# Optimization experiments

Hardware: AMD Instinct MI355X
Metric: run time of the kernel (lower is better)

The kernel has to match this reference:

```python
import math
import jax, jax.numpy as jnp
import numpy as np

B, N, CS, CZ, CH, H, PQ, PV = 1, 4096, 512, 128, 64, 16, 4, 8
BQ, BK = 32, 128
NB = N // BQ
CZ4 = CZ // 4
INF = 100000.0
EPS = 1e-8


def quat_to_rot(q):
    w, x, y, z = q[..., 0], q[..., 1], q[..., 2], q[..., 3]
    return jnp.stack([
        jnp.stack([1 - 2 * (y * y + z * z), 2 * (x * y - w * z), 2 * (x * z + w * y)], -1),
        jnp.stack([2 * (x * y + w * z), 1 - 2 * (x * x + z * z), 2 * (y * z - w * x)], -1),
        jnp.stack([2 * (x * z - w * y), 2 * (y * z + w * x), 1 - 2 * (x * x + y * y)], -1),
    ], -2)


def setup_inputs() -> dict:
    key = jax.random.key(0)
    ks = jax.random.split(key, 16)
    s = jax.random.normal(ks[0], (B, N, CS), jnp.float32)
    z = jax.random.normal(ks[1], (B, NB, BQ, BK, CZ), jnp.float32)
    trans = jax.random.normal(ks[2], (B, N, 3), jnp.float32) * 10.0
    quat = jax.random.normal(ks[3], (B, N, 4), jnp.float32)
    quat = quat / jnp.linalg.norm(quat, axis=-1, keepdims=True)
    rots = quat_to_rot(quat)
    s_mask = jnp.ones((B, N), jnp.float32)
    pad = (BK - BQ) // 2  # key window centered on each query block
    key_idx = (jnp.arange(NB)[:, None] * BQ - pad + jnp.arange(BK)[None, :]).astype(jnp.int32)

    def w(k, shp):
        return jax.random.normal(k, shp, jnp.float32) * (1.0 / math.sqrt(shp[0]))

    return {
        's': s, 'z': z, 'trans': trans, 'rots': rots, 's_mask': s_mask, 'key_idx': key_idx,
        'Wq': w(ks[4], (CS, H * CH)), 'Wk': w(ks[5], (CS, H * CH)), 'Wv': w(ks[6], (CS, H * CH)),
        'Wqp': w(ks[7], (CS, H * PQ * 3)), 'Wkvp': w(ks[8], (CS, H * (PQ + PV) * 3)),
        'Wb': w(ks[9], (CZ, H)), 'Wdz': w(ks[10], (CZ, CZ4)),
        'head_weights': jnp.full((H,), float(np.log(np.e - 1.0)), jnp.float32),  # softplus^-1(1)
        'Wout': w(ks[11], (H * (CZ4 + CH + PV * 4), CS)),
        'g_s': jnp.ones((CS,), jnp.float32), 'b_s': jnp.zeros((CS,), jnp.float32),
        'g_z': jnp.ones((CZ,), jnp.float32), 'b_z': jnp.zeros((CZ,), jnp.float32),
    }


def _ln(x, g, b):
    m = jnp.mean(x, -1, keepdims=True)
    v = jnp.mean((x - m) ** 2, -1, keepdims=True)
    return (x - m) * jax.lax.rsqrt(v + 1e-5) * g + b


def _ipa(s, z, trans, rots, s_mask, key_idx, Wq, Wk, Wv, Wqp, Wkvp, Wb, Wdz,
         head_weights, Wout, g_s, b_s, g_z, b_z):
    s_n = _ln(s, g_s, b_s)
    z_n = _ln(z, g_z, b_z)

    valid = (key_idx >= 0) & (key_idx < N)            # [NB, BK]
    idx = jnp.clip(key_idx, 0, N - 1)
    vf = valid.astype(s.dtype)[None]                  # [1, NB, BK]

    def gk(x):  # gather key window: [B,N,...] -> [B,NB,BK,...]
        return x[:, idx]

    sq = s_n.reshape(B, NB, BQ, CS)
    sk = gk(s_n) * vf[..., None]                      # zero-pad out-of-range keys

    tq = trans.reshape(B, NB, BQ, 3)
    rq = rots.reshape(B, NB, BQ, 3, 3)
    tk = gk(trans) * vf[..., None]
    rk = jnp.where(valid[None, :, :, None, None], gk(rots), jnp.eye(3, dtype=rots.dtype))

    q = (sq @ Wq).reshape(B, NB, BQ, H, CH)
    k = (sk @ Wk).reshape(B, NB, BK, H, CH)
    v = (sk @ Wv).reshape(B, NB, BK, H, CH)

    q_pts = (sq @ Wqp).reshape(B, NB, BQ, H * PQ, 3)
    q_pts = jnp.einsum('bnqij,bnqpj->bnqpi', rq, q_pts) + tq[:, :, :, None, :]
    q_pts = q_pts.reshape(B, NB, BQ, H, PQ, 3)

    kv_pts = (sk @ Wkvp).reshape(B, NB, BK, H * (PQ + PV), 3)
    kv_pts = jnp.einsum('bnkij,bnkpj->bnkpi', rk, kv_pts) + tk[:, :, :, None, :]
    kv_pts = kv_pts.reshape(B, NB, BK, H, PQ + PV, 3)
    k_pts, v_pts = kv_pts[..., :PQ, :], kv_pts[..., PQ:, :]

    bias = jnp.einsum('bnqkc,ch->bnqkh', z_n, Wb)
    a = jnp.einsum('bnqhc,bnkhc->bnqkh', q, k) * math.sqrt(1.0 / (3 * CH))
    a = a + math.sqrt(1.0 / 3) * bias

    disp = q_pts[:, :, :, None] - k_pts[:, :, None]   # [B,NB,BQ,BK,H,PQ,3]
    pt_att = jnp.sum(disp ** 2, -1)                   # [B,NB,BQ,BK,H,PQ]
    hw = jax.nn.softplus(head_weights) * math.sqrt(1.0 / (3 * (PQ * 9.0 / 2)))
    pt_att = -0.5 * jnp.sum(pt_att * hw[:, None], -1)  # [B,NB,BQ,BK,H]

    qm = s_mask.reshape(B, NB, BQ)
    km = gk(s_mask) * vf
    amask = INF * (qm[:, :, :, None] * km[:, :, None, :] - 1.0)

    a = a + pt_att + amask[..., None]
    a = jax.nn.softmax(jnp.swapaxes(a, -1, -2), axis=-1)  # [B,NB,BQ,H,BK]

    o = jnp.einsum('bnqhk,bnkhc->bnqhc', a, v).reshape(B, NB, BQ, H * CH)

    o_pt = jnp.einsum('bnqhk,bnkhpc->bnqhpc', a, v_pts)
    o_pt = jnp.einsum('bnqji,bnqhpj->bnqhpi', rq, o_pt - tq[:, :, :, None, None, :])
    o_pt_norm = jnp.sqrt(jnp.sum(o_pt ** 2, -1) + EPS).reshape(B, NB, BQ, H * PV)
    o_pt = o_pt.reshape(B, NB, BQ, H * PV * 3)

    pair_z = z_n @ Wdz                                # [B,NB,BQ,BK,CZ4]
    o_pair = jnp.einsum('bnqhk,bnqkc->bnqhc', a, pair_z).reshape(B, NB, BQ, H * CZ4)

    out = jnp.concatenate([o, o_pt, o_pt_norm, o_pair], -1) @ Wout
    return out.reshape(B, N, CS)


def reference(s, z, trans, rots, s_mask, key_idx, Wq, Wk, Wv, Wqp, Wkvp, Wb, Wdz,
              head_weights, Wout, g_s, b_s, g_z, b_z):
    return _ipa(s, z, trans, rots, s_mask, key_idx, Wq, Wk, Wv, Wqp, Wkvp, Wb, Wdz,
                head_weights, Wout, g_s, b_s, g_z, b_z)
```

## Files before the change

kernel.cpp:

```cpp
#include <hip/hip_runtime.h>
#include <math.h>

#define D_N 4096
#define PROJW 3840
#define OFFK 1024
#define OFFV 2048
#define OFFQP 3072
#define OFFKVP 3264
#define CATW 2048

typedef __bf16 bf16_t;
typedef __bf16 bf16x8 __attribute__((ext_vector_type(8)));
typedef __bf16 bf16x4 __attribute__((ext_vector_type(4)));
typedef float f32x4 __attribute__((ext_vector_type(4)));

__global__ __launch_bounds__(256) void k_wcatT(const float* __restrict__ Wq, const float* __restrict__ Wk,
    const float* __restrict__ Wv, const float* __restrict__ Wqp, const float* __restrict__ Wkvp,
    bf16_t* __restrict__ out)
{
    __shared__ float T[64][65];
    int c0 = blockIdx.x * 64;
    int r0 = blockIdx.y * 64;
    const float* src; int ld, coff;
    if (c0 < 1024)      { src = Wq;   ld = 1024; coff = c0; }
    else if (c0 < 2048) { src = Wk;   ld = 1024; coff = c0 - 1024; }
    else if (c0 < 3072) { src = Wv;   ld = 1024; coff = c0 - 2048; }
    else if (c0 < 3264) { src = Wqp;  ld = 192;  coff = c0 - 3072; }
    else                { src = Wkvp; ld = 576;  coff = c0 - 3264; }
    int tid = threadIdx.x;
    {
        int rr = tid >> 2, cb = (tid & 3) * 16;
        const float* p = src + (size_t)(r0 + rr) * ld + coff + cb;
        #pragma unroll
        for (int i = 0; i < 4; ++i)
            *(float4*)&T[rr][cb + i * 4] = *(const float4*)(p + i * 4);
    }
    __syncthreads();
    {
        int cc = tid >> 2, rb = (tid & 3) * 16;
        bf16_t* o = out + (size_t)(c0 + cc) * 512 + r0 + rb;
        bf16x8 o0, o1;
        #pragma unroll
        for (int j = 0; j < 8; ++j) o0[j] = (bf16_t)T[rb + j][cc];
        #pragma unroll
        for (int j = 0; j < 8; ++j) o1[j] = (bf16_t)T[rb + 8 + j][cc];
        *(bf16x8*)(o) = o0;
        *(bf16x8*)(o + 8) = o1;
    }
}

__global__ __launch_bounds__(256) void t_cvt(const float* __restrict__ in, bf16_t* __restrict__ out,
    int R, int C)
{
    __shared__ float T[64][65];
    int r0 = blockIdx.y * 64, c0 = blockIdx.x * 64;
    int tid = threadIdx.x;
    {
        int rr = tid >> 2;
        int cb = (tid & 3) * 16;
        const float* p = in + (size_t)(r0 + rr) * C + c0 + cb;
        #pragma unroll
        for (int i = 0; i < 4; ++i) {
            float4 v = *(const float4*)(p + i * 4);
            *(float4*)&T[rr][cb + i * 4] = v;
        }
    }
    __syncthreads();
    {
        int cc = tid >> 2;
        int rb = (tid & 3) * 16;
        bf16_t* o = out + (size_t)(c0 + cc) * R + r0 + rb;
        bf16x8 o0, o1;
        #pragma unroll
        for (int j = 0; j < 8; ++j) o0[j] = (bf16_t)T[rb + j][cc];
        #pragma unroll
        for (int j = 0; j < 8; ++j) o1[j] = (bf16_t)T[rb + 8 + j][cc];
        *(bf16x8*)(o) = o0;
        *(bf16x8*)(o + 8) = o1;
    }
}

__global__ __launch_bounds__(256) void k_wz(const float* __restrict__ Wb, const float* __restrict__ Wdz,
    bf16_t* __restrict__ WzT)
{
    int i = blockIdx.x * 256 + threadIdx.x;
    if (i >= 6144) return;
    int j = i >> 7, k = i & 127;
    float v = (j < 16) ? Wb[k * 16 + j] : Wdz[k * 32 + (j - 16)];
    WzT[i] = (bf16_t)v;
}

__global__ __launch_bounds__(64) void k_ln_s(const float* __restrict__ s, const float* __restrict__ g,
    const float* __restrict__ b, bf16_t* __restrict__ out)
{
    int row = blockIdx.x;
    int lane = threadIdx.x;
    const float4* p = (const float4*)(s + (size_t)row * 512);
    float4 v0 = p[lane];
    float4 v1 = p[lane + 64];
    float sum = v0.x + v0.y + v0.z + v0.w + v1.x + v1.y + v1.z + v1.w;
    float sq  = v0.x*v0.x + v0.y*v0.y + v0.z*v0.z + v0.w*v0.w
              + v1.x*v1.x + v1.y*v1.y + v1.z*v1.z + v1.w*v1.w;
    #pragma unroll
    for (int off = 1; off < 64; off <<= 1) {
        sum += __shfl_xor(sum, off);
        sq  += __shfl_xor(sq, off);
    }
    float m = sum * (1.0f / 512.0f);
    float var = sq * (1.0f / 512.0f) - m * m;
    float rs = rsqrtf(var + 1e-5f);
    int c = lane * 4;
    int c2 = 256 + lane * 4;
    bf16x4 r0, r1;
    r0[0] = (bf16_t)((v0.x - m) * rs * g[c+0] + b[c+0]);
    r0[1] = (bf16_t)((v0.y - m) * rs * g[c+1] + b[c+1]);
    r0[2] = (bf16_t)((v0.z - m) * rs * g[c+2] + b[c+2]);
    r0[3] = (bf16_t)((v0.w - m) * rs * g[c+3] + b[c+3]);
    r1[0] = (bf16_t)((v1.x - m) * rs * g[c2+0] + b[c2+0]);
    r1[1] = (bf16_t)((v1.y - m) * rs * g[c2+1] + b[c2+1]);
    r1[2] = (bf16_t)((v1.z - m) * rs * g[c2+2] + b[c2+2]);
    r1[3] = (bf16_t)((v1.w - m) * rs * g[c2+3] + b[c2+3]);
    *(bf16x4*)(out + (size_t)row * 512 + c)  = r0;
    *(bf16x4*)(out + (size_t)row * 512 + c2) = r1;
}

__global__ __launch_bounds__(256) void gemm_bf128(const bf16_t* __restrict__ A, const bf16_t* __restrict__ BT,
    float* __restrict__ C, int M, int N, int K)
{
    __shared__ bf16_t As[128][40];
    __shared__ bf16_t Bs[128][40];
    const int tid = threadIdx.x, lane = tid & 63, w = tid >> 6;
    const int row0 = blockIdx.y * 128, col0 = blockIdx.x * 128;
    const int wr = (w >> 1) * 64, wc = (w & 1) * 64;
    const int srow = tid >> 1, skoff = (tid & 1) * 16;
    const bf16_t* Ap = A + (size_t)(row0 + srow) * K + skoff;
    const bf16_t* Bp = BT + (size_t)(col0 + srow) * K + skoff;
    f32x4 acc[4][4];
    #pragma unroll
    for (int m = 0; m < 4; ++m)
        #pragma unroll
        for (int n = 0; n < 4; ++n) acc[m][n] = (f32x4){0.f,0.f,0.f,0.f};
    for (int k0 = 0; k0 < K; k0 += 32) {
        uint4 a0 = *(const uint4*)(Ap + k0);
        uint4 a1 = *(const uint4*)(Ap + k0 + 8);
        uint4 b0 = *(const uint4*)(Bp + k0);
        uint4 b1 = *(const uint4*)(Bp + k0 + 8);
        __syncthreads();
        *(uint4*)&As[srow][skoff]     = a0;
        *(uint4*)&As[srow][skoff + 8] = a1;
        *(uint4*)&Bs[srow][skoff]     = b0;
        *(uint4*)&Bs[srow][skoff + 8] = b1;
        __syncthreads();
        bf16x8 af[4], bfr[4];
        #pragma unroll
        for (int m = 0; m < 4; ++m) af[m]  = *(const bf16x8*)&As[wr + m*16 + (lane & 15)][(lane >> 4) * 8];
        #pragma unroll
        for (int n = 0; n < 4; ++n) bfr[n] = *(const bf16x8*)&Bs[wc + n*16 + (lane & 15)][(lane >> 4) * 8];
        #pragma unroll
        for (int m = 0; m < 4; ++m)
            #pragma unroll
            for (int n = 0; n < 4; ++n)
                acc[m][n] = __builtin_amdgcn_mfma_f32_16x16x32_bf16(af[m], bfr[n], acc[m][n], 0, 0, 0);
    }
    #pragma unroll
    for (int m = 0; m < 4; ++m)
        #pragma unroll
        for (int n = 0; n < 4; ++n)
            #pragma unroll
            for (int i = 0; i < 4; ++i)
                C[(size_t)(row0 + wr + m*16 + (lane >> 4)*4 + i) * N + col0 + wc + n*16 + (lane & 15)] = acc[m][n][i];
}

__global__ __launch_bounds__(256) void gemm_bf64(const bf16_t* __restrict__ A, const bf16_t* __restrict__ BT,
    float* __restrict__ C, int M, int N, int K)
{
    __shared__ bf16_t As[128][40];
    __shared__ bf16_t Bs[64][40];
    const int tid = threadIdx.x, lane = tid & 63, w = tid >> 6;
    const int row0 = blockIdx.y * 128, col0 = blockIdx.x * 64;
    const int wr = w * 32;
    const int srow = tid >> 1, skoff = (tid & 1) * 16;
    const int brow = tid >> 2, bkoff = (tid & 3) * 8;
    const bf16_t* Ap = A + (size_t)(row0 + srow) * K + skoff;
    const bf16_t* Bp = BT + (size_t)(col0 + brow) * K + bkoff;
    f32x4 acc[2][4];
    #pragma unroll
    for (int m = 0; m < 2; ++m)
        #pragma unroll
        for (int n = 0; n < 4; ++n) acc[m][n] = (f32x4){0.f,0.f,0.f,0.f};
    for (int k0 = 0; k0 < K; k0 += 32) {
        uint4 a0 = *(const uint4*)(Ap + k0);
        uint4 a1 = *(const uint4*)(Ap + k0 + 8);
        uint4 b0 = *(const uint4*)(Bp + k0);
        __syncthreads();
        *(uint4*)&As[srow][skoff]     = a0;
        *(uint4*)&As[srow][skoff + 8] = a1;
        *(uint4*)&Bs[brow][bkoff]     = b0;
        __syncthreads();
        bf16x8 af[2], bfr[4];
        #pragma unroll
        for (int m = 0; m < 2; ++m) af[m]  = *(const bf16x8*)&As[wr + m*16 + (lane & 15)][(lane >> 4) * 8];
        #pragma unroll
        for (int n = 0; n < 4; ++n) bfr[n] = *(const bf16x8*)&Bs[n*16 + (lane & 15)][(lane >> 4) * 8];
        #pragma unroll
        for (int m = 0; m < 2; ++m)
            #pragma unroll
            for (int n = 0; n < 4; ++n)
                acc[m][n] = __builtin_amdgcn_mfma_f32_16x16x32_bf16(af[m], bfr[n], acc[m][n], 0, 0, 0);
    }
    #pragma unroll
    for (int m = 0; m < 2; ++m)
        #pragma unroll
        for (int n = 0; n < 4; ++n)
            #pragma unroll
            for (int i = 0; i < 4; ++i)
                C[(size_t)(row0 + wr + m*16 + (lane >> 4)*4 + i) * N + col0 + n*16 + (lane & 15)] = acc[m][n][i];
}

__global__ __launch_bounds__(256) void k_rot(float* __restrict__ proj, const float* __restrict__ rots,
    const float* __restrict__ trans)
{
    int row = blockIdx.x;
    int tid = threadIdx.x;
    const float* R = rots + (size_t)row * 9;
    const float* t = trans + (size_t)row * 3;
    float* base;
    if (tid < 64) base = proj + (size_t)row * PROJW + OFFQP + tid * 3;
    else          base = proj + (size_t)row * PROJW + OFFKVP + (tid - 64) * 3;
    float x = base[0], y = base[1], z = base[2];
    base[0] = R[0] * x + R[1] * y + R[2] * z + t[0];
    base[1] = R[3] * x + R[4] * y + R[5] * z + t[1];
    base[2] = R[6] * x + R[7] * y + R[8] * z + t[2];
}

__global__ __launch_bounds__(256) void k_zbias2(const float* __restrict__ z,
    const float* __restrict__ gz, const float* __restrict__ bz,
    const bf16_t* __restrict__ WzT, float* __restrict__ biasT, bf16_t* __restrict__ pzT)
{
    __shared__ float gb_s[256];
    const int tid = threadIdx.x;
    if (tid < 128) gb_s[tid] = gz[tid];
    else           gb_s[tid] = bz[tid - 128];
    const int lane = tid & 63, w = tid >> 6;
    const int r16 = lane & 15, kg = lane >> 4;
    bf16x8 bfz[3][4];
    #pragma unroll
    for (int nt = 0; nt < 3; ++nt)
        #pragma unroll
        for (int kc = 0; kc < 4; ++kc)
            bfz[nt][kc] = *(const bf16x8*)(WzT + (size_t)(nt * 16 + r16) * 128 + kc * 32 + kg * 8);
    __syncthreads();
    const int gw = blockIdx.x * 4 + w;
    const int totw = 2048 * 4;
    for (int it = 0; it < 4; ++it) {
        const int tile = gw + it * totw;
        const int z0 = tile * 16;
        const float* zp = z + (size_t)z0 * 128 + (size_t)r16 * 128 + kg * 8;
        float4 zr[4][2];
        float sum = 0.f, sq = 0.f;
        #pragma unroll
        for (int kc = 0; kc < 4; ++kc) {
            float4 a = *(const float4*)(zp + kc * 32);
            float4 b = *(const float4*)(zp + kc * 32 + 4);
            zr[kc][0] = a; zr[kc][1] = b;
            sum += a.x + a.y + a.z + a.w + b.x + b.y + b.z + b.w;
            sq  += a.x*a.x + a.y*a.y + a.z*a.z + a.w*a.w + b.x*b.x + b.y*b.y + b.z*b.z + b.w*b.w;
        }
        sum += __shfl_xor(sum, 16); sq += __shfl_xor(sq, 16);
        sum += __shfl_xor(sum, 32); sq += __shfl_xor(sq, 32);
        float m = sum * (1.0f / 128.0f);
        float var = sq * (1.0f / 128.0f) - m * m;
        float rs = rsqrtf(var + 1e-5f);
        bf16x8 af[4];
        #pragma unroll
        for (int kc = 0; kc < 4; ++kc) {
            const float* gp = &gb_s[kc * 32 + kg * 8];
            const float* bp = &gb_s[128 + kc * 32 + kg * 8];
            float4 g0 = *(const float4*)gp,     g1 = *(const float4*)(gp + 4);
            float4 b0 = *(const float4*)bp,     b1 = *(const float4*)(bp + 4);
            af[kc][0] = (bf16_t)((zr[kc][0].x - m) * rs * g0.x + b0.x);
            af[kc][1] = (bf16_t)((zr[kc][0].y - m) * rs * g0.y + b0.y);
            af[kc][2] = (bf16_t)((zr[kc][0].z - m) * rs * g0.z + b0.z);
            af[kc][3] = (bf16_t)((zr[kc][0].w - m) * rs * g0.w + b0.w);
            af[kc][4] = (bf16_t)((zr[kc][1].x - m) * rs * g1.x + b1.x);
            af[kc][5] = (bf16_t)((zr[kc][1].y - m) * rs * g1.y + b1.y);
            af[kc][6] = (bf16_t)((zr[kc][1].z - m) * rs * g1.z + b1.z);
            af[kc][7] = (bf16_t)((zr[kc][1].w - m) * rs * g1.w + b1.w);
        }
        f32x4 acc0 = (f32x4){0.f,0.f,0.f,0.f};
        f32x4 acc1 = (f32x4){0.f,0.f,0.f,0.f};
        f32x4 acc2 = (f32x4){0.f,0.f,0.f,0.f};
        #pragma unroll
        for (int kc = 0; kc < 4; ++kc) {
            acc0 = __builtin_amdgcn_mfma_f32_16x16x32_bf16(af[kc], bfz[0][kc], acc0, 0, 0, 0);
            acc1 = __builtin_amdgcn_mfma_f32_16x16x32_bf16(af[kc], bfz[1][kc], acc1, 0, 0, 0);
            acc2 = __builtin_amdgcn_mfma_f32_16x16x32_bf16(af[kc], bfz[2][kc], acc2, 0, 0, 0);
        }
        const int rowq = z0 >> 7;
        const int k0 = (z0 & 127) + kg * 4;
        float4 bw = {acc0[0], acc0[1], acc0[2], acc0[3]};
        *(float4*)&biasT[((size_t)rowq * 16 + r16) * 128 + k0] = bw;
        bf16x4 p1, p2;
        #pragma unroll
        for (int i = 0; i < 4; ++i) { p1[i] = (bf16_t)acc1[i]; p2[i] = (bf16_t)acc2[i]; }
        *(bf16x4*)&pzT[((size_t)rowq * 32 + r16) * 128 + k0] = p1;
        *(bf16x4*)&pzT[((size_t)rowq * 32 + 16 + r16) * 128 + k0] = p2;
    }
}

__global__ __launch_bounds__(256) void k_attn2(
    const float* __restrict__ proj, const float* __restrict__ biasT,
    const float* __restrict__ rots, const float* __restrict__ trans,
    const float* __restrict__ smask, const int* __restrict__ kidx,
    const float* __restrict__ hwraw, bf16_t* __restrict__ catb,
    bf16_t* __restrict__ Pbf)
{
    __shared__ __align__(16) char uni[26112];
    __shared__ float att[32][132];
    __shared__ float kp_s[128][12];
    __shared__ float qp_s[32][12];
    __shared__ bf16_t Ps[32][136];
    __shared__ float optmp[32][33];
    __shared__ float km_s[128];
    __shared__ float qm_s[32];
    __shared__ int   rows_s[128];
    __shared__ float hws_s[4];

    bf16_t (*Qs)[72]  = (bf16_t(*)[72])uni;
    bf16_t (*Ks)[72]  = (bf16_t(*)[72])(uni + 32 * 72 * 2);
    bf16_t (*Vt)[136] = (bf16_t(*)[136])uni;

    const int nblk = blockIdx.x;
    const int hg = blockIdx.y;
    const int tid = threadIdx.x;
    const int lane = tid & 63;
    const int w = tid >> 6;
    const int rowq0 = nblk * 32;

    if (tid < 128) {
        int ki = kidx[nblk * 128 + tid];
        int valid = (ki >= 0 && ki < D_N);
        int rr = ki < 0 ? 0 : (ki > D_N - 1 ? D_N - 1 : ki);
        rows_s[tid] = rr;
        km_s[tid] = valid ? smask[rr] : 0.0f;
    } else if (tid < 160) {
        qm_s[tid - 128] = smask[rowq0 + tid - 128];
    } else if (tid < 164) {
        float x = hwraw[hg * 4 + tid - 160];
        hws_s[tid - 160] = log1pf(__expf(x)) * 0.13608276348795434f;
    }

    for (int it = 0; it < 4; ++it) {
        const int h = hg * 4 + it;
        __syncthreads();
        {
            int q = tid >> 3, cg = (tid & 7) * 8;
            const float* p = proj + (size_t)(rowq0 + q) * PROJW + h * 64 + cg;
            float4 v0 = *(const float4*)p;
            float4 v1 = *(const float4*)(p + 4);
            bf16x8 o;
            o[0]=(bf16_t)v0.x; o[1]=(bf16_t)v0.y; o[2]=(bf16_t)v0.z; o[3]=(bf16_t)v0.w;
            o[4]=(bf16_t)v1.x; o[5]=(bf16_t)v1.y; o[6]=(bf16_t)v1.z; o[7]=(bf16_t)v1.w;
            *(bf16x8*)&Qs[q][cg] = o;
        }
        if (tid < 128) {
            int q = tid >> 2, dg = (tid & 3) * 3;
            const float* p = proj + (size_t)(rowq0 + q) * PROJW + OFFQP + h * 12 + dg;
            qp_s[q][dg + 0] = p[0]; qp_s[q][dg + 1] = p[1]; qp_s[q][dg + 2] = p[2];
        }
        {
            int krow = tid >> 1, cg = (tid & 1) * 32;
            const float* p = proj + (size_t)rows_s[krow] * PROJW + OFFK + h * 64 + cg;
            #pragma unroll
            for (int u = 0; u < 4; ++u) {
                float4 v0 = *(const float4*)(p + u * 8);
                float4 v1 = *(const float4*)(p + u * 8 + 4);
                bf16x8 o;
                o[0]=(bf16_t)v0.x; o[1]=(bf16_t)v0.y; o[2]=(bf16_t)v0.z; o[3]=(bf16_t)v0.w;
                o[4]=(bf16_t)v1.x; o[5]=(bf16_t)v1.y; o[6]=(bf16_t)v1.z; o[7]=(bf16_t)v1.w;
                *(bf16x8*)&Ks[krow][cg + u * 8] = o;
            }
            const float* pk = proj + (size_t)rows_s[krow] * PROJW + OFFKVP + h * 36 + (tid & 1) * 6;
            int dg = (tid & 1) * 6;
            #pragma unroll
            for (int u = 0; u < 6; ++u) kp_s[krow][dg + u] = pk[u];
        }
        __syncthreads();
        {
            #pragma unroll
            for (int j = 0; j < 4; ++j) {
                int T = w * 4 + j;
                int m = T & 1, n = T >> 1;
                f32x4 acc = (f32x4){0.f,0.f,0.f,0.f};
                #pragma unroll
                for (int kc = 0; kc < 2; ++kc) {
                    bf16x8 a = *(const bf16x8*)&Qs[m*16 + (lane & 15)][kc*32 + (lane >> 4) * 8];
                    bf16x8 b = *(const bf16x8*)&Ks[n*16 + (lane & 15)][kc*32 + (lane >> 4) * 8];
                    acc = __builtin_amdgcn_mfma_f32_16x16x32_bf16(a, b, acc, 0, 0, 0);
                }
                #pragma unroll
                for (int i = 0; i < 4; ++i)
                    att[m*16 + (lane >> 4)*4 + i][n*16 + (lane & 15)] = acc[i];
            }
        }
        __syncthreads();
        {
            int krow = tid >> 1, cg = (tid & 1) * 32;
            const float* p = proj + (size_t)rows_s[krow] * PROJW + OFFV + h * 64 + cg;
            #pragma unroll
            for (int u = 0; u < 8; ++u) {
                float4 v = *(const float4*)(p + u * 4);
                Vt[cg + u*4 + 0][krow] = (bf16_t)v.x;
                Vt[cg + u*4 + 1][krow] = (bf16_t)v.y;
                Vt[cg + u*4 + 2][krow] = (bf16_t)v.z;
                Vt[cg + u*4 + 3][krow] = (bf16_t)v.w;
            }
            const float* pv = proj + (size_t)rows_s[krow] * PROJW + OFFKVP + h * 36 + 12 + (tid & 1) * 12;
            #pragma unroll
            for (int u = 0; u < 3; ++u) {
                float4 v = *(const float4*)(pv + u * 4);
                int rb = 64 + (tid & 1) * 12 + u * 4;
                Vt[rb + 0][krow] = (bf16_t)v.x;
                Vt[rb + 1][krow] = (bf16_t)v.y;
                Vt[rb + 2][krow] = (bf16_t)v.z;
                Vt[rb + 3][krow] = (bf16_t)v.w;
            }
            {
                int r = 88 + (tid >> 5), c = (tid & 31) * 4;
                bf16x4 zz; zz[0]=(bf16_t)0.f; zz[1]=(bf16_t)0.f; zz[2]=(bf16_t)0.f; zz[3]=(bf16_t)0.f;
                *(bf16x4*)&Vt[r][c] = zz;
            }
            int q = tid >> 3, kg = tid & 7;
            float qp[12];
            #pragma unroll
            for (int e = 0; e < 12; ++e) qp[e] = qp_s[q][e];
            float qm = qm_s[q];
            float hw = hws_s[it];
            const float* bT = biasT + ((size_t)(rowq0 + q) * 16 + h) * 128;
            #pragma unroll
            for (int j2 = 0; j2 < 16; ++j2) {
                int k = kg + j2 * 8;
                float4 k0 = *(const float4*)&kp_s[k][0];
                float4 k1 = *(const float4*)&kp_s[k][4];
                float4 k2 = *(const float4*)&kp_s[k][8];
                float d0 = qp[0]-k0.x, d1 = qp[1]-k0.y, d2_ = qp[2]-k0.z, d3 = qp[3]-k0.w;
                float d4 = qp[4]-k1.x, d5 = qp[5]-k1.y, d6 = qp[6]-k1.z, d7 = qp[7]-k1.w;
                float d8 = qp[8]-k2.x, d9 = qp[9]-k2.y, d10 = qp[10]-k2.z, d11 = qp[11]-k2.w;
                float dd = d0*d0+d1*d1+d2_*d2_+d3*d3+d4*d4+d5*d5+d6*d6+d7*d7+d8*d8+d9*d9+d10*d10+d11*d11;
                float val = att[q][k] * 0.07216878364870323f
                          + 0.5773502691896258f * bT[k]
                          + 100000.0f * (qm * km_s[k] - 1.0f)
                          - 0.5f * hw * dd;
                att[q][k] = val;
            }
        }
        __syncthreads();
        {
            int q = tid >> 3, kg = tid & 7;
            float l[16];
            #pragma unroll
            for (int j2 = 0; j2 < 16; ++j2) l[j2] = att[q][kg + j2 * 8];
            float mx = l[0];
            #pragma unroll
            for (int j2 = 1; j2 < 16; ++j2) mx = fmaxf(mx, l[j2]);
            mx = fmaxf(mx, __shfl_xor(mx, 1));
            mx = fmaxf(mx, __shfl_xor(mx, 2));
            mx = fmaxf(mx, __shfl_xor(mx, 4));
            float se = 0.f;
            #pragma unroll
            for (int j2 = 0; j2 < 16; ++j2) { l[j2] = __expf(l[j2] - mx); se += l[j2]; }
            se += __shfl_xor(se, 1);
            se += __shfl_xor(se, 2);
            se += __shfl_xor(se, 4);
            float inv = 1.0f / se;
            bf16_t* pg = Pbf + ((size_t)(rowq0 + q) * 16 + h) * 128;
            #pragma unroll
            for (int j2 = 0; j2 < 16; ++j2) {
                bf16_t pb = (bf16_t)(l[j2] * inv);
                Ps[q][kg + j2 * 8] = pb;
                pg[kg + j2 * 8] = pb;
            }
        }
        __syncthreads();
        {
            #pragma unroll
            for (int j = 0; j < 3; ++j) {
                int T = w * 3 + j;
                int m = T & 1, n = T >> 1;
                f32x4 acc = (f32x4){0.f,0.f,0.f,0.f};
                #pragma unroll
                for (int kc = 0; kc < 4; ++kc) {
                    bf16x8 a = *(const bf16x8*)&Ps[m*16 + (lane & 15)][kc*32 + (lane >> 4) * 8];
                    bf16x8 b = *(const bf16x8*)&Vt[n*16 + (lane & 15)][kc*32 + (lane >> 4) * 8];
                    acc = __builtin_amdgcn_mfma_f32_16x16x32_bf16(a, b, acc, 0, 0, 0);
                }
                int rowb = m * 16 + (lane >> 4) * 4;
                int col = lane & 15;
                if (n < 4) {
                    #pragma unroll
                    for (int i = 0; i < 4; ++i)
                        catb[(size_t)(rowq0 + rowb + i) * CATW + h * 64 + n * 16 + col] = (bf16_t)acc[i];
                } else {
                    #pragma unroll
                    for (int i = 0; i < 4; ++i)
                        optmp[rowb + i][(n - 4) * 16 + col] = acc[i];
                }
            }
        }
        __syncthreads();
        {
            int q = tid >> 3, pp = tid & 7;
            float sx = optmp[q][pp * 3 + 0];
            float sy = optmp[q][pp * 3 + 1];
            float sz = optmp[q][pp * 3 + 2];
            const float* R = rots + (size_t)(rowq0 + q) * 9;
            const float* t = trans + (size_t)(rowq0 + q) * 3;
            float x = sx - t[0], y = sy - t[1], z2 = sz - t[2];
            float ox = R[0] * x + R[3] * y + R[6] * z2;
            float oy = R[1] * x + R[4] * y + R[7] * z2;
            float oz = R[2] * x + R[5] * y + R[8] * z2;
            bf16_t* cp = catb + (size_t)(rowq0 + q) * CATW;
            cp[1024 + h * 24 + pp * 3 + 0] = (bf16_t)ox;
            cp[1024 + h * 24 + pp * 3 + 1] = (bf16_t)oy;
            cp[1024 + h * 24 + pp * 3 + 2] = (bf16_t)oz;
            cp[1408 + h * 8 + pp] = (bf16_t)sqrtf(ox * ox + oy * oy + oz * oz + 1e-8f);
        }
    }
}

__global__ __launch_bounds__(256) void k_opair(const bf16_t* __restrict__ Pbf,
    const bf16_t* __restrict__ pzT, bf16_t* __restrict__ catb)
{
    int tid = threadIdx.x, lane = tid & 63, w = tid >> 6;
    size_t rowq = (size_t)blockIdx.x * 4 + w;
    const bf16_t* Pp = Pbf + rowq * 2048;
    const bf16_t* zp = pzT + rowq * 4096;
    bf16x8 pa[4];
    #pragma unroll
    for (int kc = 0; kc < 4; ++kc)
        pa[kc] = *(const bf16x8*)(Pp + (size_t)(lane & 15) * 128 + kc * 32 + (lane >> 4) * 8);
    #pragma unroll
    for (int ct = 0; ct < 2; ++ct) {
        f32x4 acc = (f32x4){0.f,0.f,0.f,0.f};
        #pragma unroll
        for (int kc = 0; kc < 4; ++kc) {
            bf16x8 b = *(const bf16x8*)(zp + (size_t)(ct * 16 + (lane & 15)) * 128 + kc * 32 + (lane >> 4) * 8);
            acc = __builtin_amdgcn_mfma_f32_16x16x32_bf16(pa[kc], b, acc, 0, 0, 0);
        }
        #pragma unroll
        for (int i = 0; i < 4; ++i) {
            int hh = (lane >> 4) * 4 + i;
            catb[rowq * CATW + 1536 + hh * 32 + ct * 16 + (lane & 15)] = (bf16_t)acc[i];
        }
    }
}

extern "C" void kernel_launch(void* const* d_in, const int* in_sizes, int n_in,
                              void* d_out, int out_size, void* d_ws, size_t ws_size,
                              hipStream_t stream)
{
    (void)in_sizes; (void)n_in; (void)out_size;
    const float* s     = (const float*)d_in[0];
    const float* z     = (const float*)d_in[1];
    const float* trans = (const float*)d_in[2];
    const float* rots  = (const float*)d_in[3];
    const float* smask = (const float*)d_in[4];
    const int*   kidx  = (const int*)d_in[5];
    const float* Wq    = (const float*)d_in[6];
    const float* Wk    = (const float*)d_in[7];
    const float* Wv    = (const float*)d_in[8];
    const float* Wqp   = (const float*)d_in[9];
    const float* Wkvp  = (const float*)d_in[10];
    const float* Wb    = (const float*)d_in[11];
    const float* Wdz   = (const float*)d_in[12];
    const float* hw    = (const float*)d_in[13];
    const float* Wout  = (const float*)d_in[14];
    const float* g_s   = (const float*)d_in[15];
    const float* b_s   = (const float*)d_in[16];
    const float* g_z   = (const float*)d_in[17];
    const float* b_z   = (const float*)d_in[18];

    char* ws = (char*)d_ws;
    float*  proj  = (float*)(ws);
    float*  biasT = (float*)(ws + 70778880);
    bf16_t* wcatT = (bf16_t*)(ws + 104333312);
    bf16_t* s_nb  = (bf16_t*)(ws + 108265472);
    bf16_t* pzT   = (bf16_t*)(ws + 112459776);
    bf16_t* Pbf   = (bf16_t*)(ws + 146014208);
    bf16_t* catb  = (bf16_t*)(ws + 162791424);
    bf16_t* WoutT = (bf16_t*)(ws + 179568640);
    bf16_t* WzT   = (bf16_t*)(ws + 181665792);
    if (ws_size < (size_t)181678080) return;
    float* out = (float*)d_out;

    k_wcatT<<<dim3(60, 8), 256, 0, stream>>>(Wq, Wk, Wv, Wqp, Wkvp, wcatT);
    t_cvt<<<dim3(8, 32), 256, 0, stream>>>(Wout, WoutT, 2048, 512);
    k_wz<<<24, 256, 0, stream>>>(Wb, Wdz, WzT);
    k_ln_s<<<4096, 64, 0, stream>>>(s, g_s, b_s, s_nb);
    gemm_bf128<<<dim3(30, 32), 256, 0, stream>>>(s_nb, wcatT, proj, 4096, 3840, 512);
    k_rot<<<4096, 256, 0, stream>>>(proj, rots, trans);
    k_zbias2<<<2048, 256, 0, stream>>>(z, g_z, b_z, WzT, biasT, pzT);
    k_attn2<<<dim3(128, 4), 256, 0, stream>>>(proj, biasT, rots, trans, smask, kidx, hw, catb, Pbf);
    k_opair<<<1024, 256, 0, stream>>>(Pbf, pzT, catb);
    gemm_bf64<<<dim3(8, 32), 256, 0, stream>>>(catb, WoutT, out, 4096, 512, 2048);
}
```

Before: 249.9 us.

## Split projections into bf16/f32 buffers, fold z-LN affine into weights, async-load z

The projection GEMM now writes Q/K/V in bf16 and only the point projections in f32, which shrinks the intermediate and lets the attention kernel load bf16 directly. The z layer-norm gain and bias are folded into the pair weights plus a precomputed constant vector. The z-bias kernel stages z through LDS with global_load_lds double buffering. Attention is launched with one head per block (16 blocks in y) instead of looping four heads. Rounding Q/K/V to bf16 earlier and the manual vmcnt waits add precision and correctness risk.

```diff
diff --git a/kernel.cpp b/kernel.cpp
--- a/kernel.cpp
+++ b/kernel.cpp
@@ -2,17 +2,21 @@
 #include <math.h>
 
 #define D_N 4096
-#define PROJW 3840
+#define PBW 3072
+#define PPW 768
 #define OFFK 1024
 #define OFFV 2048
-#define OFFQP 3072
-#define OFFKVP 3264
 #define CATW 2048
 
 typedef __bf16 bf16_t;
 typedef __bf16 bf16x8 __attribute__((ext_vector_type(8)));
 typedef __bf16 bf16x4 __attribute__((ext_vector_type(4)));
 typedef float f32x4 __attribute__((ext_vector_type(4)));
+
+__device__ __forceinline__ void gld16(const void* g, void* l) {
+    __builtin_amdgcn_global_load_lds((const __attribute__((address_space(1))) unsigned int*)g,
+                                     (__attribute__((address_space(3))) unsigned int*)l, 16, 0, 0);
+}
 
 __global__ __launch_bounds__(256) void k_wcatT(const float* __restrict__ Wq, const float* __restrict__ Wk,
     const float* __restrict__ Wv, const float* __restrict__ Wqp, const float* __restrict__ Wkvp,
@@ -80,14 +84,25 @@
     }
 }
 
-__global__ __launch_bounds__(256) void k_wz(const float* __restrict__ Wb, const float* __restrict__ Wdz,
-    bf16_t* __restrict__ WzT)
+__global__ __launch_bounds__(256) void k_wz2(const float* __restrict__ Wb, const float* __restrict__ Wdz,
+    const float* __restrict__ gz, const float* __restrict__ bz,
+    bf16_t* __restrict__ WzT, float* __restrict__ Kv)
 {
     int i = blockIdx.x * 256 + threadIdx.x;
-    if (i >= 6144) return;
-    int j = i >> 7, k = i & 127;
-    float v = (j < 16) ? Wb[k * 16 + j] : Wdz[k * 32 + (j - 16)];
-    WzT[i] = (bf16_t)v;
+    if (i < 6144) {
+        int j = i >> 7, c = i & 127;
+        float w = (j < 16) ? Wb[c * 16 + j] : Wdz[c * 32 + (j - 16)];
+        WzT[i] = (bf16_t)(gz[c] * w);
+    }
+    if (blockIdx.x == 0 && threadIdx.x < 48) {
+        int j = threadIdx.x;
+        float acc = 0.f;
+        for (int c = 0; c < 128; ++c) {
+            float w = (j < 16) ? Wb[c * 16 + j] : Wdz[c * 32 + (j - 16)];
+            acc += bz[c] * w;
+        }
+        Kv[j] = acc;
+    }
 }
 
 __global__ __launch_bounds__(64) void k_ln_s(const float* __restrict__ s, const float* __restrict__ g,
@@ -124,8 +139,8 @@
     *(bf16x4*)(out + (size_t)row * 512 + c2) = r1;
 }
 
-__global__ __launch_bounds__(256) void gemm_bf128(const bf16_t* __restrict__ A, const bf16_t* __restrict__ BT,
-    float* __restrict__ C, int M, int N, int K)
+__global__ __launch_bounds__(256) void gemm_proj(const bf16_t* __restrict__ A, const bf16_t* __restrict__ BT,
+    bf16_t* __restrict__ projb, float* __restrict__ projp, int K)
 {
     __shared__ bf16_t As[128][40];
     __shared__ bf16_t Bs[128][40];
@@ -162,13 +177,25 @@
             for (int n = 0; n < 4; ++n)
                 acc[m][n] = __builtin_amdgcn_mfma_f32_16x16x32_bf16(af[m], bfr[n], acc[m][n], 0, 0, 0);
     }
-    #pragma unroll
-    for (int m = 0; m < 4; ++m)
-        #pragma unroll
-        for (int n = 0; n < 4; ++n)
-            #pragma unroll
-            for (int i = 0; i < 4; ++i)
-                C[(size_t)(row0 + wr + m*16 + (lane >> 4)*4 + i) * N + col0 + wc + n*16 + (lane & 15)] = acc[m][n][i];
+    if (col0 < 3072) {
+        #pragma unroll
+        for (int m = 0; m < 4; ++m)
+            #pragma unroll
+            for (int n = 0; n < 4; ++n)
+                #pragma unroll
+                for (int i = 0; i < 4; ++i)
+                    projb[(size_t)(row0 + wr + m*16 + (lane >> 4)*4 + i) * PBW + col0 + wc + n*16 + (lane & 15)]
+                        = (bf16_t)acc[m][n][i];
+    } else {
+        #pragma unroll
+        for (int m = 0; m < 4; ++m)
+            #pragma unroll
+            for (int n = 0; n < 4; ++n)
+                #pragma unroll
+                for (int i = 0; i < 4; ++i)
+                    projp[(size_t)(row0 + wr + m*16 + (lane >> 4)*4 + i) * PPW + col0 - 3072 + wc + n*16 + (lane & 15)]
+                        = acc[m][n][i];
+    }
 }
 
 __global__ __launch_bounds__(256) void gemm_bf64(const bf16_t* __restrict__ A, const bf16_t* __restrict__ BT,
@@ -217,31 +244,26 @@
                 C[(size_t)(row0 + wr + m*16 + (lane >> 4)*4 + i) * N + col0 + n*16 + (lane & 15)] = acc[m][n][i];
 }
 
-__global__ __launch_bounds__(256) void k_rot(float* __restrict__ proj, const float* __restrict__ rots,
+__global__ __launch_bounds__(256) void k_rot(float* __restrict__ projp, const float* __restrict__ rots,
     const float* __restrict__ trans)
 {
     int row = blockIdx.x;
     int tid = threadIdx.x;
     const float* R = rots + (size_t)row * 9;
     const float* t = trans + (size_t)row * 3;
-    float* base;
-    if (tid < 64) base = proj + (size_t)row * PROJW + OFFQP + tid * 3;
-    else          base = proj + (size_t)row * PROJW + OFFKVP + (tid - 64) * 3;
+    float* base = projp + (size_t)row * PPW + tid * 3;
     float x = base[0], y = base[1], z = base[2];
     base[0] = R[0] * x + R[1] * y + R[2] * z + t[0];
     base[1] = R[3] * x + R[4] * y + R[5] * z + t[1];
     base[2] = R[6] * x + R[7] * y + R[8] * z + t[2];
 }
 
-__global__ __launch_bounds__(256) void k_zbias2(const float* __restrict__ z,
-    const float* __restrict__ gz, const float* __restrict__ bz,
-    const bf16_t* __restrict__ WzT, float* __restrict__ biasT, bf16_t* __restrict__ pzT)
-{
-    __shared__ float gb_s[256];
-    const int tid = threadIdx.x;
-    if (tid < 128) gb_s[tid] = gz[tid];
-    else           gb_s[tid] = bz[tid - 128];
-    const int lane = tid & 63, w = tid >> 6;
+__global__ __launch_bounds__(256) void k_zbias3(const float* __restrict__ z,
+    const bf16_t* __restrict__ WzT, const float* __restrict__ Kv,
+    float* __restrict__ biasT, bf16_t* __restrict__ pzT)
+{
+    __shared__ __align__(16) float zbuf[2][64][128];
+    const int tid = threadIdx.x, lane = tid & 63, w = tid >> 6;
     const int r16 = lane & 15, kg = lane >> 4;
     bf16x8 bfz[3][4];
     #pragma unroll
@@ -249,71 +271,89 @@
         #pragma unroll
         for (int kc = 0; kc < 4; ++kc)
             bfz[nt][kc] = *(const bf16x8*)(WzT + (size_t)(nt * 16 + r16) * 128 + kc * 32 + kg * 8);
-    __syncthreads();
-    const int gw = blockIdx.x * 4 + w;
-    const int totw = 2048 * 4;
-    for (int it = 0; it < 4; ++it) {
-        const int tile = gw + it * totw;
-        const int z0 = tile * 16;
-        const float* zp = z + (size_t)z0 * 128 + (size_t)r16 * 128 + kg * 8;
-        float4 zr[4][2];
-        float sum = 0.f, sq = 0.f;
-        #pragma unroll
-        for (int kc = 0; kc < 4; ++kc) {
-            float4 a = *(const float4*)(zp + kc * 32);
-            float4 b = *(const float4*)(zp + kc * 32 + 4);
-            zr[kc][0] = a; zr[kc][1] = b;
-            sum += a.x + a.y + a.z + a.w + b.x + b.y + b.z + b.w;
-            sq  += a.x*a.x + a.y*a.y + a.z*a.z + a.w*a.w + b.x*b.x + b.y*b.y + b.z*b.z + b.w*b.w;
-        }
-        sum += __shfl_xor(sum, 16); sq += __shfl_xor(sq, 16);
-        sum += __shfl_xor(sum, 32); sq += __shfl_xor(sq, 32);
-        float m = sum * (1.0f / 128.0f);
-        float var = sq * (1.0f / 128.0f) - m * m;
-        float rs = rsqrtf(var + 1e-5f);
-        bf16x8 af[4];
-        #pragma unroll
-        for (int kc = 0; kc < 4; ++kc) {
-            const float* gp = &gb_s[kc * 32 + kg * 8];
-            const float* bp = &gb_s[128 + kc * 32 + kg * 8];
-            float4 g0 = *(const float4*)gp,     g1 = *(const float4*)(gp + 4);
-            float4 b0 = *(const float4*)bp,     b1 = *(const float4*)(bp + 4);
-            af[kc][0] = (bf16_t)((zr[kc][0].x - m) * rs * g0.x + b0.x);
-            af[kc][1] = (bf16_t)((zr[kc][0].y - m) * rs * g0.y + b0.y);
-            af[kc][2] = (bf16_t)((zr[kc][0].z - m) * rs * g0.z + b0.z);
-            af[kc][3] = (bf16_t)((zr[kc][0].w - m) * rs * g0.w + b0.w);
-            af[kc][4] = (bf16_t)((zr[kc][1].x - m) * rs * g1.x + b1.x);
-            af[kc][5] = (bf16_t)((zr[kc][1].y - m) * rs * g1.y + b1.y);
-            af[kc][6] = (bf16_t)((zr[kc][1].z - m) * rs * g1.z + b1.z);
-            af[kc][7] = (bf16_t)((zr[kc][1].w - m) * rs * g1.w + b1.w);
-        }
-        f32x4 acc0 = (f32x4){0.f,0.f,0.f,0.f};
-        f32x4 acc1 = (f32x4){0.f,0.f,0.f,0.f};
-        f32x4 acc2 = (f32x4){0.f,0.f,0.f,0.f};
-        #pragma unroll
-        for (int kc = 0; kc < 4; ++kc) {
-            acc0 = __builtin_amdgcn_mfma_f32_16x16x32_bf16(af[kc], bfz[0][kc], acc0, 0, 0, 0);
-            acc1 = __builtin_amdgcn_mfma_f32_16x16x32_bf16(af[kc], bfz[1][kc], acc1, 0, 0, 0);
-            acc2 = __builtin_amdgcn_mfma_f32_16x16x32_bf16(af[kc], bfz[2][kc], acc2, 0, 0, 0);
-        }
-        const int rowq = z0 >> 7;
-        const int k0 = (z0 & 127) + kg * 4;
-        float4 bw = {acc0[0], acc0[1], acc0[2], acc0[3]};
-        *(float4*)&biasT[((size_t)rowq * 16 + r16) * 128 + k0] = bw;
-        bf16x4 p1, p2;
-        #pragma unroll
-        for (int i = 0; i < 4; ++i) { p1[i] = (bf16_t)acc1[i]; p2[i] = (bf16_t)acc2[i]; }
-        *(bf16x4*)&pzT[((size_t)rowq * 32 + r16) * 128 + k0] = p1;
-        *(bf16x4*)&pzT[((size_t)rowq * 32 + 16 + r16) * 128 + k0] = p2;
-    }
-}
-
-__global__ __launch_bounds__(256) void k_attn2(
-    const float* __restrict__ proj, const float* __restrict__ biasT,
-    const float* __restrict__ rots, const float* __restrict__ trans,
-    const float* __restrict__ smask, const int* __restrict__ kidx,
-    const float* __restrict__ hwraw, bf16_t* __restrict__ catb,
-    bf16_t* __restrict__ Pbf)
+    float K0 = Kv[r16], K1 = Kv[16 + r16], K2 = Kv[32 + r16];
+    asm volatile("s_waitcnt vmcnt(0)" ::: "memory");
+
+    const int gid = blockIdx.x * 4 + w;
+    const char* zb = (const char*)z + (size_t)gid * 64 * 512;
+    char* lb0 = (char*)&zbuf[0][w * 16][0];
+    char* lb1 = (char*)&zbuf[1][w * 16][0];
+
+#define STAGE(i, lb) { \
+    const char* gp_ = zb + (size_t)(i) * 8192 + lane * 16; \
+    _Pragma("unroll") \
+    for (int c_ = 0; c_ < 8; ++c_) gld16(gp_ + c_ * 1024, (lb) + c_ * 1024); }
+
+#define PROCESS(i, b) { \
+    const float* rp = &zbuf[b][w * 16 + r16][kg * 8]; \
+    float4 za[4], zc[4]; \
+    float sum = 0.f, sq = 0.f; \
+    _Pragma("unroll") \
+    for (int kc = 0; kc < 4; ++kc) { \
+        float4 a_ = *(const float4*)(rp + kc * 32); \
+        float4 b_ = *(const float4*)(rp + kc * 32 + 4); \
+        za[kc] = a_; zc[kc] = b_; \
+        sum += a_.x + a_.y + a_.z + a_.w + b_.x + b_.y + b_.z + b_.w; \
+        sq  += a_.x*a_.x + a_.y*a_.y + a_.z*a_.z + a_.w*a_.w + b_.x*b_.x + b_.y*b_.y + b_.z*b_.z + b_.w*b_.w; \
+    } \
+    sum += __shfl_xor(sum, 16); sq += __shfl_xor(sq, 16); \
+    sum += __shfl_xor(sum, 32); sq += __shfl_xor(sq, 32); \
+    float m_ = sum * (1.0f / 128.0f); \
+    float rs_ = rsqrtf(sq * (1.0f / 128.0f) - m_ * m_ + 1e-5f); \
+    bf16x8 af[4]; \
+    _Pragma("unroll") \
+    for (int kc = 0; kc < 4; ++kc) { \
+        af[kc][0] = (bf16_t)((za[kc].x - m_) * rs_); \
+        af[kc][1] = (bf16_t)((za[kc].y - m_) * rs_); \
+        af[kc][2] = (bf16_t)((za[kc].z - m_) * rs_); \
+        af[kc][3] = (bf16_t)((za[kc].w - m_) * rs_); \
+        af[kc][4] = (bf16_t)((zc[kc].x - m_) * rs_); \
+        af[kc][5] = (bf16_t)((zc[kc].y - m_) * rs_); \
+        af[kc][6] = (bf16_t)((zc[kc].z - m_) * rs_); \
+        af[kc][7] = (bf16_t)((zc[kc].w - m_) * rs_); \
+    } \
+    f32x4 acc0 = (f32x4){0.f,0.f,0.f,0.f}; \
+    f32x4 acc1 = (f32x4){0.f,0.f,0.f,0.f}; \
+    f32x4 acc2 = (f32x4){0.f,0.f,0.f,0.f}; \
+    _Pragma("unroll") \
+    for (int kc = 0; kc < 4; ++kc) { \
+        acc0 = __builtin_amdgcn_mfma_f32_16x16x32_bf16(af[kc], bfz[0][kc], acc0, 0, 0, 0); \
+        acc1 = __builtin_amdgcn_mfma_f32_16x16x32_bf16(af[kc], bfz[1][kc], acc1, 0, 0, 0); \
+        acc2 = __builtin_amdgcn_mfma_f32_16x16x32_bf16(af[kc], bfz[2][kc], acc2, 0, 0, 0); \
+    } \
+    const int t_ = gid * 4 + (i); \
+    const int rowq_ = t_ >> 3; \
+    const int k0_ = ((t_ & 7) << 4) + kg * 4; \
+    float4 bw = {acc0[0] + K0, acc0[1] + K0, acc0[2] + K0, acc0[3] + K0}; \
+    *(float4*)&biasT[((size_t)rowq_ * 16 + r16) * 128 + k0_] = bw; \
+    bf16x4 p1, p2; \
+    _Pragma("unroll") \
+    for (int i2 = 0; i2 < 4; ++i2) { p1[i2] = (bf16_t)(acc1[i2] + K1); p2[i2] = (bf16_t)(acc2[i2] + K2); } \
+    *(bf16x4*)&pzT[((size_t)rowq_ * 32 + r16) * 128 + k0_] = p1; \
+    *(bf16x4*)&pzT[((size_t)rowq_ * 32 + 16 + r16) * 128 + k0_] = p2; }
+
+    STAGE(0, lb0);
+    STAGE(1, lb1);
+    asm volatile("s_waitcnt vmcnt(8)" ::: "memory");
+    PROCESS(0, 0);
+    STAGE(2, lb0);
+    asm volatile("s_waitcnt vmcnt(11)" ::: "memory");
+    PROCESS(1, 1);
+    STAGE(3, lb1);
+    asm volatile("s_waitcnt vmcnt(11)" ::: "memory");
+    PROCESS(2, 0);
+    asm volatile("s_waitcnt vmcnt(3)" ::: "memory");
+    PROCESS(3, 1);
+#undef STAGE
+#undef PROCESS
+}
+
+__global__ __launch_bounds__(256) void k_attn3(
+    const bf16_t* __restrict__ projb, const float* __restrict__ projp,
+    const float* __restrict__ biasT, const float* __restrict__ rots,
+    const float* __restrict__ trans, const float* __restrict__ smask,
+    const int* __restrict__ kidx, const float* __restrict__ hwraw,
+    bf16_t* __restrict__ catb, bf16_t* __restrict__ Pbf)
 {
     __shared__ __align__(16) char uni[26112];
     __shared__ float att[32][132];
@@ -324,18 +364,18 @@
     __shared__ float km_s[128];
     __shared__ float qm_s[32];
     __shared__ int   rows_s[128];
-    __shared__ float hws_s[4];
 
     bf16_t (*Qs)[72]  = (bf16_t(*)[72])uni;
     bf16_t (*Ks)[72]  = (bf16_t(*)[72])(uni + 32 * 72 * 2);
     bf16_t (*Vt)[136] = (bf16_t(*)[136])uni;
 
     const int nblk = blockIdx.x;
-    const int hg = blockIdx.y;
+    const int h = blockIdx.y;
     const int tid = threadIdx.x;
     const int lane = tid & 63;
     const int w = tid >> 6;
     const int rowq0 = nblk * 32;
+    const float hw = log1pf(__expf(hwraw[h])) * 0.13608276348795434f;
 
     if (tid < 128) {
         int ki = kidx[nblk * 128 + tid];
@@ -345,186 +385,164 @@
         km_s[tid] = valid ? smask[rr] : 0.0f;
     } else if (tid < 160) {
         qm_s[tid - 128] = smask[rowq0 + tid - 128];
-    } else if (tid < 164) {
-        float x = hwraw[hg * 4 + tid - 160];
-        hws_s[tid - 160] = log1pf(__expf(x)) * 0.13608276348795434f;
-    }
-
-    for (int it = 0; it < 4; ++it) {
-        const int h = hg * 4 + it;
-        __syncthreads();
+    }
+    __syncthreads();
+    {
+        int q = tid >> 3, cg = (tid & 7) * 8;
+        *(bf16x8*)&Qs[q][cg] = *(const bf16x8*)(projb + (size_t)(rowq0 + q) * PBW + h * 64 + cg);
+    }
+    if (tid < 128) {
+        int q = tid >> 2, dg = (tid & 3) * 3;
+        const float* p = projp + (size_t)(rowq0 + q) * PPW + h * 12 + dg;
+        qp_s[q][dg + 0] = p[0]; qp_s[q][dg + 1] = p[1]; qp_s[q][dg + 2] = p[2];
+    }
+    {
+        int krow = tid >> 1, cg = (tid & 1) * 32;
+        const bf16_t* p = projb + (size_t)rows_s[krow] * PBW + OFFK + h * 64 + cg;
+        #pragma unroll
+        for (int u = 0; u < 4; ++u)
+            *(bf16x8*)&Ks[krow][cg + u * 8] = *(const bf16x8*)(p + u * 8);
+        const float* pk = projp + (size_t)rows_s[krow] * PPW + 192 + h * 36 + (tid & 1) * 6;
+        int dg = (tid & 1) * 6;
+        #pragma unroll
+        for (int u = 0; u < 6; ++u) kp_s[krow][dg + u] = pk[u];
+    }
+    __syncthreads();
+    {
+        #pragma unroll
+        for (int j = 0; j < 4; ++j) {
+            int T = w * 4 + j;
+            int m = T & 1, n = T >> 1;
+            f32x4 acc = (f32x4){0.f,0.f,0.f,0.f};
+            #pragma unroll
+            for (int kc = 0; kc < 2; ++kc) {
+                bf16x8 a = *(const bf16x8*)&Qs[m*16 + (lane & 15)][kc*32 + (lane >> 4) * 8];
+                bf16x8 b = *(const bf16x8*)&Ks[n*16 + (lane & 15)][kc*32 + (lane >> 4) * 8];
+                acc = __builtin_amdgcn_mfma_f32_16x16x32_bf16(a, b, acc, 0, 0, 0);
+            }
+            #pragma unroll
+            for (int i = 0; i < 4; ++i)
+                att[m*16 + (lane >> 4)*4 + i][n*16 + (lane & 15)] = acc[i];
+        }
+    }
+    __syncthreads();
+    {
+        int krow = tid >> 1, cg = (tid & 1) * 32;
+        const bf16_t* p = projb + (size_t)rows_s[krow] * PBW + OFFV + h * 64 + cg;
+        #pragma unroll
+        for (int u4 = 0; u4 < 4; ++u4) {
+            bf16x8 v = *(const bf16x8*)(p + u4 * 8);
+            #pragma unroll
+            for (int j = 0; j < 8; ++j) Vt[cg + u4 * 8 + j][krow] = v[j];
+        }
+        const float* pv = projp + (size_t)rows_s[krow] * PPW + 192 + h * 36 + 12 + (tid & 1) * 12;
+        #pragma unroll
+        for (int u = 0; u < 3; ++u) {
+            float4 v = *(const float4*)(pv + u * 4);
+            int rb = 64 + (tid & 1) * 12 + u * 4;
+            Vt[rb + 0][krow] = (bf16_t)v.x;
+            Vt[rb + 1][krow] = (bf16_t)v.y;
+            Vt[rb + 2][krow] = (bf16_t)v.z;
+            Vt[rb + 3][krow] = (bf16_t)v.w;
+        }
         {
-            int q = tid >> 3, cg = (tid & 7) * 8;
-            const float* p = proj + (size_t)(rowq0 + q) * PROJW + h * 64 + cg;
-            float4 v0 = *(const float4*)p;
-            float4 v1 = *(const float4*)(p + 4);
-            bf16x8 o;
-            o[0]=(bf16_t)v0.x; o[1]=(bf16_t)v0.y; o[2]=(bf16_t)v0.z; o[3]=(bf16_t)v0.w;
-            o[4]=(bf16_t)v1.x; o[5]=(bf16_t)v1.y; o[6]=(bf16_t)v1.z; o[7]=(bf16_t)v1.w;
-            *(bf16x8*)&Qs[q][cg] = o;
-        }
-        if (tid < 128) {
-            int q = tid >> 2, dg = (tid & 3) * 3;
-            const float* p = proj + (size_t)(rowq0 + q) * PROJW + OFFQP + h * 12 + dg;
-            qp_s[q][dg + 0] = p[0]; qp_s[q][dg + 1] = p[1]; qp_s[q][dg + 2] = p[2];
-        }
-        {
-            int krow = tid >> 1, cg = (tid & 1) * 32;
-            const float* p = proj + (size_t)rows_s[krow] * PROJW + OFFK + h * 64 + cg;
-            #pragma unroll
-            for (int u = 0; u < 4; ++u) {
-                float4 v0 = *(const float4*)(p + u * 8);
-                float4 v1 = *(const float4*)(p + u * 8 + 4);
-                bf16x8 o;
-                o[0]=(bf16_t)v0.x; o[1]=(bf16_t)v0.y; o[2]=(bf16_t)v0.z; o[3]=(bf16_t)v0.w;
-                o[4]=(bf16_t)v1.x; o[5]=(bf16_t)v1.y; o[6]=(bf16_t)v1.z; o[7]=(bf16_t)v1.w;
-                *(bf16x8*)&Ks[krow][cg + u * 8] = o;
+            int r = 88 + (tid >> 5), c = (tid & 31) * 4;
+            bf16x4 zz; zz[0]=(bf16_t)0.f; zz[1]=(bf16_t)0.f; zz[2]=(bf16_t)0.f; zz[3]=(bf16_t)0.f;
+            *(bf16x4*)&Vt[r][c] = zz;
+        }
+        int q = tid >> 3, kg = tid & 7;
+        float qp[12];
+        #pragma unroll
+        for (int e = 0; e < 12; ++e) qp[e] = qp_s[q][e];
+        float qm = qm_s[q];
+        const float* bT = biasT + ((size_t)(rowq0 + q) * 16 + h) * 128;
+        #pragma unroll
+        for (int j2 = 0; j2 < 16; ++j2) {
+            int k = kg + j2 * 8;
+            float4 k0 = *(const float4*)&kp_s[k][0];
+            float4 k1 = *(const float4*)&kp_s[k][4];
+            float4 k2 = *(const float4*)&kp_s[k][8];
+            float d0 = qp[0]-k0.x, d1 = qp[1]-k0.y, d2_ = qp[2]-k0.z, d3 = qp[3]-k0.w;
+            float d4 = qp[4]-k1.x, d5 = qp[5]-k1.y, d6 = qp[6]-k1.z, d7 = qp[7]-k1.w;
+            float d8 = qp[8]-k2.x, d9 = qp[9]-k2.y, d10 = qp[10]-k2.z, d11 = qp[11]-k2.w;
+            float dd = d0*d0+d1*d1+d2_*d2_+d3*d3+d4*d4+d5*d5+d6*d6+d7*d7+d8*d8+d9*d9+d10*d10+d11*d11;
+            float val = att[q][k] * 0.07216878364870323f
+                      + 0.5773502691896258f * bT[k]
+                      + 100000.0f * (qm * km_s[k] - 1.0f)
+                      - 0.5f * hw * dd;
+            att[q][k] = val;
+        }
+    }
+    __syncthreads();
+    {
+        int q = tid >> 3, kg = tid & 7;
+        float l[16];
+        #pragma unroll
+        for (int j2 = 0; j2 < 16; ++j2) l[j2] = att[q][kg + j2 * 8];
+        float mx = l[0];
+        #pragma unroll
+        for (int j2 = 1; j2 < 16; ++j2) mx = fmaxf(mx, l[j2]);
+        mx = fmaxf(mx, __shfl_xor(mx, 1));
+        mx = fmaxf(mx, __shfl_xor(mx, 2));
+        mx = fmaxf(mx, __shfl_xor(mx, 4));
+        float se = 0.f;
+        #pragma unroll
+        for (int j2 = 0; j2 < 16; ++j2) { l[j2] = __expf(l[j2] - mx); se += l[j2]; }
+        se += __shfl_xor(se, 1);
+        se += __shfl_xor(se, 2);
+        se += __shfl_xor(se, 4);
+        float inv = 1.0f / se;
+        bf16_t* pg = Pbf + ((size_t)(rowq0 + q) * 16 + h) * 128;
+        #pragma unroll
+        for (int j2 = 0; j2 < 16; ++j2) {
+            bf16_t pb = (bf16_t)(l[j2] * inv);
+            Ps[q][kg + j2 * 8] = pb;
+            pg[kg + j2 * 8] = pb;
+        }
+    }
+    __syncthreads();
+    {
+        #pragma unroll
+        for (int j = 0; j < 3; ++j) {
+            int T = w * 3 + j;
+            int m = T & 1, n = T >> 1;
+            f32x4 acc = (f32x4){0.f,0.f,0.f,0.f};
+            #pragma unroll
+            for (int kc = 0; kc < 4; ++kc) {
+                bf16x8 a = *(const bf16x8*)&Ps[m*16 + (lane & 15)][kc*32 + (lane >> 4) * 8];
+                bf16x8 b = *(const bf16x8*)&Vt[n*16 + (lane & 15)][kc*32 + (lane >> 4) * 8];
+                acc = __builtin_amdgcn_mfma_f32_16x16x32_bf16(a, b, acc, 0, 0, 0);
             }
-            const float* pk = proj + (size_t)rows_s[krow] * PROJW + OFFKVP + h * 36 + (tid & 1) * 6;
-            int dg = (tid & 1) * 6;
-            #pragma unroll
-            for (int u = 0; u < 6; ++u) kp_s[krow][dg + u] = pk[u];
-        }
-        __syncthreads();
-        {
-            #pragma unroll
-            for (int j = 0; j < 4; ++j) {
-                int T = w * 4 + j;
-                int m = T & 1, n = T >> 1;
-                f32x4 acc = (f32x4){0.f,0.f,0.f,0.f};
-                #pragma unroll
-                for (int kc = 0; kc < 2; ++kc) {
-                    bf16x8 a = *(const bf16x8*)&Qs[m*16 + (lane & 15)][kc*32 + (lane >> 4) * 8];
-                    bf16x8 b = *(const bf16x8*)&Ks[n*16 + (lane & 15)][kc*32 + (lane >> 4) * 8];
-                    acc = __builtin_amdgcn_mfma_f32_16x16x32_bf16(a, b, acc, 0, 0, 0);
-                }
+            int rowb = m * 16 + (lane >> 4) * 4;
+            int col = lane & 15;
+            if (n < 4) {
                 #pragma unroll
                 for (int i = 0; i < 4; ++i)
-                    att[m*16 + (lane >> 4)*4 + i][n*16 + (lane & 15)] = acc[i];
+                    catb[(size_t)(rowq0 + rowb + i) * CATW + h * 64 + n * 16 + col] = (bf16_t)acc[i];
+            } else {
+                #pragma unroll
+                for (int i = 0; i < 4; ++i)
+                    optmp[rowb + i][(n - 4) * 16 + col] = acc[i];
             }
         }
-        __syncthreads();
-        {
-            int krow = tid >> 1, cg = (tid & 1) * 32;
-            const float* p = proj + (size_t)rows_s[krow] * PROJW + OFFV + h * 64 + cg;
-            #pragma unroll
-            for (int u = 0; u < 8; ++u) {
-                float4 v = *(const float4*)(p + u * 4);
-                Vt[cg + u*4 + 0][krow] = (bf16_t)v.x;
-                Vt[cg + u*4 + 1][krow] = (bf16_t)v.y;
-                Vt[cg + u*4 + 2][krow] = (bf16_t)v.z;
-                Vt[cg + u*4 + 3][krow] = (bf16_t)v.w;
-            }
-            const float* pv = proj + (size_t)rows_s[krow] * PROJW + OFFKVP + h * 36 + 12 + (tid & 1) * 12;
-            #pragma unroll
-            for (int u = 0; u < 3; ++u) {
-                float4 v = *(const float4*)(pv + u * 4);
-                int rb = 64 + (tid & 1) * 12 + u * 4;
-                Vt[rb + 0][krow] = (bf16_t)v.x;
-                Vt[rb + 1][krow] = (bf16_t)v.y;
-                Vt[rb + 2][krow] = (bf16_t)v.z;
-                Vt[rb + 3][krow] = (bf16_t)v.w;
-            }
-            {
-                int r = 88 + (tid >> 5), c = (tid & 31) * 4;
-                bf16x4 zz; zz[0]=(bf16_t)0.f; zz[1]=(bf16_t)0.f; zz[2]=(bf16_t)0.f; zz[3]=(bf16_t)0.f;
-                *(bf16x4*)&Vt[r][c] = zz;
-            }
-            int q = tid >> 3, kg = tid & 7;
-            float qp[12];
-            #pragma unroll
-            for (int e = 0; e < 12; ++e) qp[e] = qp_s[q][e];
-            float qm = qm_s[q];
-            float hw = hws_s[it];
-            const float* bT = biasT + ((size_t)(rowq0 + q) * 16 + h) * 128;
-            #pragma unroll
-            for (int j2 = 0; j2 < 16; ++j2) {
-                int k = kg + j2 * 8;
-                float4 k0 = *(const float4*)&kp_s[k][0];
-                float4 k1 = *(const float4*)&kp_s[k][4];
-                float4 k2 = *(const float4*)&kp_s[k][8];
-                float d0 = qp[0]-k0.x, d1 = qp[1]-k0.y, d2_ = qp[2]-k0.z, d3 = qp[3]-k0.w;
-                float d4 = qp[4]-k1.x, d5 = qp[5]-k1.y, d6 = qp[6]-k1.z, d7 = qp[7]-k1.w;
-                float d8 = qp[8]-k2.x, d9 = qp[9]-k2.y, d10 = qp[10]-k2.z, d11 = qp[11]-k2.w;
-                float dd = d0*d0+d1*d1+d2_*d2_+d3*d3+d4*d4+d5*d5+d6*d6+d7*d7+d8*d8+d9*d9+d10*d10+d11*d11;
-                float val = att[q][k] * 0.07216878364870323f
-                          + 0.5773502691896258f * bT[k]
-                          + 100000.0f * (qm * km_s[k] - 1.0f)
-                          - 0.5f * hw * dd;
-                att[q][k] = val;
-            }
-        }
-        __syncthreads();
-        {
-            int q = tid >> 3, kg = tid & 7;
-            float l[16];
-            #pragma unroll
-            for (int j2 = 0; j2 < 16; ++j2) l[j2] = att[q][kg + j2 * 8];
-            float mx = l[0];
-            #pragma unroll
-            for (int j2 = 1; j2 < 16; ++j2) mx = fmaxf(mx, l[j2]);
-            mx = fmaxf(mx, __shfl_xor(mx, 1));
-            mx = fmaxf(mx, __shfl_xor(mx, 2));
-            mx = fmaxf(mx, __shfl_xor(mx, 4));
-            float se = 0.f;
-            #pragma unroll
-            for (int j2 = 0; j2 < 16; ++j2) { l[j2] = __expf(l[j2] - mx); se += l[j2]; }
-            se += __shfl_xor(se, 1);
-            se += __shfl_xor(se, 2);
-            se += __shfl_xor(se, 4);
-            float inv = 1.0f / se;
-            bf16_t* pg = Pbf + ((size_t)(rowq0 + q) * 16 + h) * 128;
-            #pragma unroll
-            for (int j2 = 0; j2 < 16; ++j2) {
-                bf16_t pb = (bf16_t)(l[j2] * inv);
-                Ps[q][kg + j2 * 8] = pb;
-                pg[kg + j2 * 8] = pb;
-            }
-        }
-        __syncthreads();
-        {
-            #pragma unroll
-            for (int j = 0; j < 3; ++j) {
-                int T = w * 3 + j;
-                int m = T & 1, n = T >> 1;
-                f32x4 acc = (f32x4){0.f,0.f,0.f,0.f};
-                #pragma unroll
-                for (int kc = 0; kc < 4; ++kc) {
-                    bf16x8 a = *(const bf16x8*)&Ps[m*16 + (lane & 15)][kc*32 + (lane >> 4) * 8];
-                    bf16x8 b = *(const bf16x8*)&Vt[n*16 + (lane & 15)][kc*32 + (lane >> 4) * 8];
-                    acc = __builtin_amdgcn_mfma_f32_16x16x32_bf16(a, b, acc, 0, 0, 0);
-                }
-                int rowb = m * 16 + (lane >> 4) * 4;
-                int col = lane & 15;
-                if (n < 4) {
-                    #pragma unroll
-                    for (int i = 0; i < 4; ++i)
-                        catb[(size_t)(rowq0 + rowb + i) * CATW + h * 64 + n * 16 + col] = (bf16_t)acc[i];
-                } else {
-                    #pragma unroll
-                    for (int i = 0; i < 4; ++i)
-                        optmp[rowb + i][(n - 4) * 16 + col] = acc[i];
-                }
-            }
-        }
-        __syncthreads();
-        {
-            int q = tid >> 3, pp = tid & 7;
-            float sx = optmp[q][pp * 3 + 0];
-            float sy = optmp[q][pp * 3 + 1];
-            float sz = optmp[q][pp * 3 + 2];
-            const float* R = rots + (size_t)(rowq0 + q) * 9;
-            const float* t = trans + (size_t)(rowq0 + q) * 3;
-            float x = sx - t[0], y = sy - t[1], z2 = sz - t[2];
-            float ox = R[0] * x + R[3] * y + R[6] * z2;
-            float oy = R[1] * x + R[4] * y + R[7] * z2;
-            float oz = R[2] * x + R[5] * y + R[8] * z2;
-            bf16_t* cp = catb + (size_t)(rowq0 + q) * CATW;
-            cp[1024 + h * 24 + pp * 3 + 0] = (bf16_t)ox;
-            cp[1024 + h * 24 + pp * 3 + 1] = (bf16_t)oy;
-            cp[1024 + h * 24 + pp * 3 + 2] = (bf16_t)oz;
-            cp[1408 + h * 8 + pp] = (bf16_t)sqrtf(ox * ox + oy * oy + oz * oz + 1e-8f);
-        }
+    }
+    __syncthreads();
+    {
+        int q = tid >> 3, pp = tid & 7;
+        float sx = optmp[q][pp * 3 + 0];
+        float sy = optmp[q][pp * 3 + 1];
+        float sz = optmp[q][pp * 3 + 2];
+        const float* R = rots + (size_t)(rowq0 + q) * 9;
+        const float* t = trans + (size_t)(rowq0 + q) * 3;
+        float x = sx - t[0], y = sy - t[1], z2 = sz - t[2];
+        float ox = R[0] * x + R[3] * y + R[6] * z2;
+        float oy = R[1] * x + R[4] * y + R[7] * z2;
+        float oz = R[2] * x + R[5] * y + R[8] * z2;
+        bf16_t* cp = catb + (size_t)(rowq0 + q) * CATW;
+        cp[1024 + h * 24 + pp * 3 + 0] = (bf16_t)ox;
+        cp[1024 + h * 24 + pp * 3 + 1] = (bf16_t)oy;
+        cp[1024 + h * 24 + pp * 3 + 2] = (bf16_t)oz;
+        cp[1408 + h * 8 + pp] = (bf16_t)sqrtf(ox * ox + oy * oy + oz * oz + 1e-8f);
     }
 }
 
@@ -581,26 +599,28 @@
     const float* b_z   = (const float*)d_in[18];
 
     char* ws = (char*)d_ws;
-    float*  proj  = (float*)(ws);
-    float*  biasT = (float*)(ws + 70778880);
-    bf16_t* wcatT = (bf16_t*)(ws + 104333312);
-    bf16_t* s_nb  = (bf16_t*)(ws + 108265472);
-    bf16_t* pzT   = (bf16_t*)(ws + 112459776);
-    bf16_t* Pbf   = (bf16_t*)(ws + 146014208);
-    bf16_t* catb  = (bf16_t*)(ws + 162791424);
-    bf16_t* WoutT = (bf16_t*)(ws + 179568640);
-    bf16_t* WzT   = (bf16_t*)(ws + 181665792);
-    if (ws_size < (size_t)181678080) return;
+    bf16_t* projb = (bf16_t*)(ws);
+    float*  projp = (float*)(ws + 25165824);
+    float*  biasT = (float*)(ws + 37748736);
+    bf16_t* wcatT = (bf16_t*)(ws + 71303168);
+    bf16_t* s_nb  = (bf16_t*)(ws + 75235328);
+    bf16_t* pzT   = (bf16_t*)(ws + 79429632);
+    bf16_t* Pbf   = (bf16_t*)(ws + 112984064);
+    bf16_t* catb  = (bf16_t*)(ws + 129761280);
+    bf16_t* WoutT = (bf16_t*)(ws + 146538496);
+    bf16_t* WzT   = (bf16_t*)(ws + 148635648);
+    float*  Kv    = (float*)(ws + 148647936);
+    if (ws_size < (size_t)148648128) return;
     float* out = (float*)d_out;
 
     k_wcatT<<<dim3(60, 8), 256, 0, stream>>>(Wq, Wk, Wv, Wqp, Wkvp, wcatT);
     t_cvt<<<dim3(8, 32), 256, 0, stream>>>(Wout, WoutT, 2048, 512);
-    k_wz<<<24, 256, 0, stream>>>(Wb, Wdz, WzT);
+    k_wz2<<<24, 256, 0, stream>>>(Wb, Wdz, g_z, b_z, WzT, Kv);
     k_ln_s<<<4096, 64, 0, stream>>>(s, g_s, b_s, s_nb);
-    gemm_bf128<<<dim3(30, 32), 256, 0, stream>>>(s_nb, wcatT, proj, 4096, 3840, 512);
-    k_rot<<<4096, 256, 0, stream>>>(proj, rots, trans);
-    k_zbias2<<<2048, 256, 0, stream>>>(z, g_z, b_z, WzT, biasT, pzT);
-    k_attn2<<<dim3(128, 4), 256, 0, stream>>>(proj, biasT, rots, trans, smask, kidx, hw, catb, Pbf);
+    gemm_proj<<<dim3(30, 32), 256, 0, stream>>>(s_nb, wcatT, projb, projp, 512);
+    k_rot<<<4096, 256, 0, stream>>>(projp, rots, trans);
+    k_zbias3<<<2048, 256, 0, stream>>>(z, WzT, Kv, biasT, pzT);
+    k_attn3<<<dim3(128, 16), 256, 0, stream>>>(projb, projp, biasT, rots, trans, smask, kidx, hw, catb, Pbf);
     k_opair<<<1024, 256, 0, stream>>>(Pbf, pzT, catb);
     gemm_bf64<<<dim3(8, 32), 256, 0, stream>>>(catb, WoutT, out, 4096, 512, 2048);
 }
```

Result: faster. 237.3 us (-5.1%).
